# Performance work log

Measured on AMD Instinct MI355X. Metric: run time of the kernel, lower is better.

The kernel has to match this reference:

```python
import jax, jax.numpy as jnp
import numpy as np

K_NEIGHBORS = 6
LN_EPS = 1e-5


def _layernorm(h, g, b):
    m = h.mean(-1, keepdims=True)
    v = h.var(-1, keepdims=True)
    return (h - m) / jnp.sqrt(v + LN_EPS) * g + b


def _mlp(h, w0, b0, w1, b1):
    return jax.nn.relu(h @ w0 + b0) @ w1 + b1


def _learn_adj(x, Wp, bp):
    # EfficientGraphStructureLearner: cosine-sim topk graph, symmetrized, row-normalized
    h = x @ Wp + bp
    nrm = jnp.linalg.norm(h, axis=1, keepdims=True)
    h = h / jnp.maximum(nrm, 1e-12)
    S = h @ h.T                                  # [N, N]
    vals, idx = jax.lax.top_k(S, K_NEIGHBORS + 1)  # col 0 is self (diag == 1)
    N = x.shape[0]
    rows = jnp.arange(N)[:, None]
    adj = jnp.zeros_like(S).at[rows, idx[:, 1:]].set(vals[:, 1:])
    adj = (adj + adj.T) * 0.5
    adj = adj / (adj.sum(1, keepdims=True) + 1e-8)
    return adj


def _gcn(h, adj, W, b):
    # StandardGraphConv: D^-1/2 (A+I) D^-1/2 @ (h W) + b (diag matmuls as row/col scaling)
    A = adj + jnp.eye(adj.shape[0], dtype=adj.dtype)
    d = jnp.maximum(A.sum(1), 1e-12) ** -0.5
    norm_adj = d[:, None] * A * d[None, :]
    return norm_adj @ (h @ W) + b


def setup_inputs() -> dict:
    key = jax.random.key(0)
    ks = iter(jax.random.split(key, 40))
    N, D, H, O, HP = 8192, 20, 32, 128, 16
    f = lambda *s: jax.random.normal(next(ks), s, dtype=jnp.float32) * 0.1
    inp = {
        'x': jax.random.normal(next(ks), (N, D), dtype=jnp.float32),
        'Wp': f(D, HP), 'bp': jnp.zeros((HP,), jnp.float32),
        'gw0': f(D, H), 'gb0': jnp.zeros((H,), jnp.float32),
        'gw1': f(H, H), 'gb1': jnp.zeros((H,), jnp.float32),
        'gw2': f(H, O), 'gb2': jnp.zeros((O,), jnp.float32),
        'lg0': jnp.ones((H,), jnp.float32), 'lb0': jnp.zeros((H,), jnp.float32),
        'lg1': jnp.ones((H,), jnp.float32), 'lb1': jnp.zeros((H,), jnp.float32),
        'lg2': jnp.ones((O,), jnp.float32), 'lb2': jnp.zeros((O,), jnp.float32),
        'riw0': f(D, H), 'rib0': jnp.zeros((H,), jnp.float32),
        'riw1': f(H, H), 'rib1': jnp.zeros((H,), jnp.float32),
        'rhw0': f(H, H), 'rhb0': jnp.zeros((H,), jnp.float32),
        'rhw1': f(H, H), 'rhb1': jnp.zeros((H,), jnp.float32),
        'row0': f(H, O), 'rob0': jnp.zeros((O,), jnp.float32),
        'row1': f(O, O), 'rob1': jnp.zeros((O,), jnp.float32),
    }
    return inp


def reference(x, Wp, bp, gw0, gb0, gw1, gb1, gw2, gb2,
              lg0, lb0, lg1, lb1, lg2, lb2,
              riw0, rib0, riw1, rib1,
              rhw0, rhb0, rhw1, rhb1,
              row0, rob0, row1, rob1):
    adj = _learn_adj(x, Wp, bp)
    gcns = [(gw0, gb0, lg0, lb0), (gw1, gb1, lg1, lb1), (gw2, gb2, lg2, lb2)]
    skips = [(riw0, rib0, riw1, rib1), (rhw0, rhb0, rhw1, rhb1), (row0, rob0, row1, rob1)]
    h = x
    for i, ((W, b, g, bt), sk) in enumerate(zip(gcns, skips)):
        h_new = jax.nn.relu(_layernorm(_gcn(h, adj, W, b), g, bt))
        h = h_new + _mlp(h, *sk)
        # dropout is identity in eval mode
    return h
```

## Files before the change

### kernel.cpp

```cpp
#include <hip/hip_runtime.h>

constexpr int D_IN = 20;
constexpr int HP   = 16;
constexpr int K    = 6;
constexpr int SAMP = 512;
constexpr int CAPL = 384;
constexpr int CIN  = 128;
constexpr float MARGIN = 0.01f;

typedef __attribute__((ext_vector_type(8))) short bf16x8;
typedef __attribute__((ext_vector_type(4))) float f32x4;

__device__ __forceinline__ float dot16_seq(const float4* q, const float4* c) {
  float s = 0.f;
#pragma unroll
  for (int m = 0; m < 4; ++m) {
    s = fmaf(q[m].x, c[m].x, s);
    s = fmaf(q[m].y, c[m].y, s);
    s = fmaf(q[m].z, c[m].z, s);
    s = fmaf(q[m].w, c[m].w, s);
  }
  return s;
}

__device__ __forceinline__ short f2bf(float f) {
  unsigned u = __float_as_uint(f);
  unsigned r = (u + 0x7fffu + ((u >> 16) & 1u)) >> 16;
  return (short)r;
}

__device__ __forceinline__ float dinv_of(float own, float ins) {
  float rs = 0.5f * (own + ins);
  float rn = 1.f / (rs + 1e-8f);
  return rsqrtf(fmaxf(1.f + rs * rn, 1e-12f));
}

__global__ void k_proj(const float* __restrict__ x, const float* __restrict__ Wp,
                       const float* __restrict__ bp, const float* __restrict__ gw0,
                       float* __restrict__ hn, short* __restrict__ hnb,
                       float* __restrict__ XW0,
                       float* __restrict__ insum, int* __restrict__ indeg, int N) {
  int i = blockIdx.x * blockDim.x + threadIdx.x;
  if (i >= N) return;
  insum[i] = 0.f; indeg[i] = 0;
  float xr[D_IN];
#pragma unroll
  for (int d = 0; d < D_IN; ++d) xr[d] = x[i*D_IN + d];
  float hv[HP];
  float nrm2 = 0.f;
#pragma unroll
  for (int h = 0; h < HP; ++h) {
    float a = bp[h];
#pragma unroll
    for (int d = 0; d < D_IN; ++d) a += xr[d] * Wp[d*HP + h];
    hv[h] = a;
    nrm2 += a * a;
  }
  float inv = 1.f / fmaxf(sqrtf(nrm2), 1e-12f);
#pragma unroll
  for (int h = 0; h < HP; ++h) {
    float v = hv[h] * inv;
    hn[i*HP + h] = v;
    hnb[(size_t)i*32 + h] = f2bf(v);
  }
#pragma unroll
  for (int h = 0; h < HP; ++h) hnb[(size_t)i*32 + 16 + h] = 0;
#pragma unroll
  for (int oc = 0; oc < 32; ++oc) {
    float a = 0.f;
#pragma unroll
    for (int d = 0; d < D_IN; ++d) a += xr[d] * gw0[d*32 + oc];
    XW0[(size_t)i*32 + oc] = a;
  }
}

struct Top6 { float v0,v1,v2,v3,v4,v5; int i0,i1,i2,i3,i4,i5; };

__device__ __forceinline__ void t6_init(Top6& t) {
  t.v0=t.v1=t.v2=t.v3=t.v4=t.v5=-1e30f;
  t.i0=t.i1=t.i2=t.i3=t.i4=t.i5=-1;
}

#define T6_SWAP(a,b,ia,ib) { float tv=a; a=b; b=tv; int ti=ia; ia=ib; ib=ti; }

__device__ __forceinline__ void t6_insert(Top6& t, float s, int c) {
  if (s > t.v5) {
    t.v5 = s; t.i5 = c;
    if (t.v5 > t.v4) { T6_SWAP(t.v4, t.v5, t.i4, t.i5); }
    if (t.v4 > t.v3) { T6_SWAP(t.v3, t.v4, t.i3, t.i4); }
    if (t.v3 > t.v2) { T6_SWAP(t.v2, t.v3, t.i2, t.i3); }
    if (t.v2 > t.v1) { T6_SWAP(t.v1, t.v2, t.i1, t.i2); }
    if (t.v1 > t.v0) { T6_SWAP(t.v0, t.v1, t.i0, t.i1); }
  }
}

__device__ __forceinline__ void t6_best(const Top6& t, float& cv, int& ci) {
  cv = t.v0; ci = t.i0;
  if (t.v1 > cv || (t.v1 == cv && (unsigned)t.i1 < (unsigned)ci)) { cv = t.v1; ci = t.i1; }
  if (t.v2 > cv || (t.v2 == cv && (unsigned)t.i2 < (unsigned)ci)) { cv = t.v2; ci = t.i2; }
  if (t.v3 > cv || (t.v3 == cv && (unsigned)t.i3 < (unsigned)ci)) { cv = t.v3; ci = t.i3; }
  if (t.v4 > cv || (t.v4 == cv && (unsigned)t.i4 < (unsigned)ci)) { cv = t.v4; ci = t.i4; }
  if (t.v5 > cv || (t.v5 == cv && (unsigned)t.i5 < (unsigned)ci)) { cv = t.v5; ci = t.i5; }
}

__device__ __forceinline__ void t6_consume(Top6& t, int mi) {
  if (t.i0 == mi) t.v0 = -1e30f;
  if (t.i1 == mi) t.v1 = -1e30f;
  if (t.i2 == mi) t.v2 = -1e30f;
  if (t.i3 == mi) t.v3 = -1e30f;
  if (t.i4 == mi) t.v4 = -1e30f;
  if (t.i5 == mi) t.v5 = -1e30f;
}

__global__ __launch_bounds__(256) void k_thresh(const float* __restrict__ hn,
                                                float* __restrict__ tau, int N) {
  int wave = threadIdx.x >> 6, lane = threadIdx.x & 63;
  int row = blockIdx.x * 4 + wave;
  const float4* hn4 = (const float4*)hn;
  float4 q[4];
#pragma unroll
  for (int m = 0; m < 4; ++m) q[m] = hn4[(size_t)row*4 + m];
  Top6 t; t6_init(t);
#pragma unroll
  for (int k = 0; k < SAMP/64; ++k) {
    int c = lane + 64*k;
    if (c != row) {
      float4 cv[4];
#pragma unroll
      for (int m = 0; m < 4; ++m) cv[m] = hn4[(size_t)c*4 + m];
      float s = dot16_seq(q, cv);
      t6_insert(t, s, c);
    }
  }
  float last = -1e30f;
  for (int sel = 0; sel < K; ++sel) {
    float cv; int ci;
    t6_best(t, cv, ci);
    float mv = cv; int mi = ci;
#pragma unroll
    for (int m = 1; m < 64; m <<= 1) {
      float ov = __shfl_xor(mv, m);
      int   oi = __shfl_xor(mi, m);
      if (ov > mv || (ov == mv && (unsigned)oi < (unsigned)mi)) { mv = ov; mi = oi; }
    }
    t6_consume(t, mi);
    last = mv;
  }
  if (lane == 0) tau[row] = last;
}

__global__ __launch_bounds__(1024) void k_scan23(
    const float* __restrict__ hn, const short* __restrict__ hnb,
    const float* __restrict__ tau,
    float* __restrict__ evals, int* __restrict__ eidx,
    float* __restrict__ ownsum, float* insum, int* indeg,
    unsigned short* __restrict__ incol, float* __restrict__ inval, int N) {
  __shared__ unsigned short hbuf[16][CAPL];
  __shared__ int cntl[16];
  int tid = threadIdx.x;
  int wave = tid >> 6, lane = tid & 63;
  int r0 = blockIdx.x * 16;
  const float4* hn4 = (const float4*)hn;

  if (tid < 16) cntl[tid] = 0;
  __syncthreads();

  {
    int half = lane >> 4;
    int l16  = lane & 15;
    int gleader = half << 4;
    unsigned below = (1u << l16) - 1u;
    bf16x8 a = *(const bf16x8*)(hnb + (size_t)(r0 + l16)*32 + half*8);
    float4 t4 = *(const float4*)(tau + r0 + half*4);
    float tm0 = t4.x - MARGIN, tm1 = t4.y - MARGIN,
          tm2 = t4.z - MARGIN, tm3 = t4.w - MARGIN;
    f32x4 zero = {0.f, 0.f, 0.f, 0.f};
    const int SPANW = N / 16;
    int jb0 = wave * SPANW;

#define APPB2(R, HA, HB)                                                     \
    {                                                                        \
      bool hA = (HA), hB = (HB);                                             \
      unsigned long long mrA = __ballot(hA);                                 \
      unsigned long long mrB = __ballot(hB);                                 \
      unsigned maskA = (unsigned)(mrA >> (16*half)) & 0xFFFFu;               \
      unsigned maskB = (unsigned)(mrB >> (16*half)) & 0xFFFFu;               \
      if (maskA | maskB) {                                                   \
        int rl = 4*half + (R);                                               \
        int pca = __popc(maskA);                                             \
        int base = 0;                                                        \
        if (l16 == 0) base = atomicAdd(&cntl[rl], pca + __popc(maskB));      \
        base = __shfl(base, gleader);                                        \
        if (hA) {                                                            \
          int p = base + __popc(maskA & below);                              \
          if (p < CAPL) hbuf[rl][p] = (unsigned short)(jbA + l16);           \
        }                                                                    \
        if (hB) {                                                            \
          int p = base + pca + __popc(maskB & below);                        \
          if (p < CAPL) hbuf[rl][p] = (unsigned short)(jbB + l16);           \
        }                                                                    \
      }                                                                      \
    }

#pragma unroll 2
    for (int jt = 0; jt < SPANW; jt += 32) {
      int jbA = jb0 + jt, jbB = jbA + 16;
      bf16x8 bA = *(const bf16x8*)(hnb + (size_t)(jbA + l16)*32 + half*8);
      bf16x8 bB = *(const bf16x8*)(hnb + (size_t)(jbB + l16)*32 + half*8);
      f32x4 dA = __builtin_amdgcn_mfma_f32_16x16x32_bf16(a, bA, zero, 0, 0, 0);
      f32x4 dB = __builtin_amdgcn_mfma_f32_16x16x32_bf16(a, bB, zero, 0, 0, 0);
      bool a0 = dA[0] >= tm0, a1 = dA[1] >= tm1, a2 = dA[2] >= tm2, a3 = dA[3] >= tm3;
      bool b0 = dB[0] >= tm0, b1 = dB[1] >= tm1, b2 = dB[2] >= tm2, b3 = dB[3] >= tm3;
      if (__any(a0 | a1 | a2 | a3 | b0 | b1 | b2 | b3)) {
        APPB2(0, a0, b0) APPB2(1, a1, b1) APPB2(2, a2, b2) APPB2(3, a3, b3)
      }
    }
#undef APPB2
  }
  __syncthreads();

  {
    int row = r0 + wave;
    int n = min(cntl[wave], CAPL);
    float4 q[4];
#pragma unroll
    for (int m = 0; m < 4; ++m) q[m] = hn4[(size_t)row*4 + m];
    Top6 t; t6_init(t);
    for (int e = lane; e < n; e += 64) {
      int j = hbuf[wave][e];
      if (j != row) {
        float4 cv[4];
#pragma unroll
        for (int m = 0; m < 4; ++m) cv[m] = hn4[(size_t)j*4 + m];
        float sc = dot16_seq(q, cv);
        t6_insert(t, sc, j);
      }
    }
    float osum = 0.f;
    for (int sel = 0; sel < K; ++sel) {
      float cv; int ci;
      t6_best(t, cv, ci);
      float mv = cv; int mi = ci;
#pragma unroll
      for (int m = 1; m < 64; m <<= 1) {
        float ov = __shfl_xor(mv, m);
        int   oi = __shfl_xor(mi, m);
        if (ov > mv || (ov == mv && (unsigned)oi < (unsigned)mi)) { mv = ov; mi = oi; }
      }
      t6_consume(t, mi);
      if (lane == 0) {
        evals[row*K + sel] = mv;
        eidx [row*K + sel] = mi;
        osum += mv;
        atomicAdd(&insum[mi], mv);
        int pos = atomicAdd(&indeg[mi], 1);
        if (pos < CIN) {
          incol[(size_t)mi*CIN + pos] = (unsigned short)row;
          inval[(size_t)mi*CIN + pos] = mv;
        }
      }
    }
    if (lane == 0) ownsum[row] = osum;
  }
}

template<int DIN, int NEXTD, bool SCALED>
__global__ __launch_bounds__(256) void k_gpost32(
    const float* __restrict__ XWsrc,
    const int* __restrict__ eidx, const float* __restrict__ evals,
    const unsigned short* __restrict__ incol, const float* __restrict__ inval,
    const int* __restrict__ indeg,
    const float* __restrict__ ownsum, const float* __restrict__ insum,
    const float* __restrict__ gb, const float* __restrict__ lg, const float* __restrict__ lb,
    const float* __restrict__ hprev,
    const float* __restrict__ w0, const float* __restrict__ b0,
    const float* __restrict__ w1, const float* __restrict__ b1,
    const float* __restrict__ Wnext, float* __restrict__ XWnext,
    float* __restrict__ outp, int N) {
  __shared__ float hid[4][2][32];
  int tid = threadIdx.x;
  int lane = tid & 63, wslot = tid >> 6;
  int sub = lane >> 5, ol = lane & 31;
  int row = (blockIdx.x * 4 + wslot) * 2 + sub;

  float rs_i = 0.5f * (ownsum[row] + insum[row]);
  float rn_i = 1.f / (rs_i + 1e-8f);
  float di_i = rsqrtf(fmaxf(1.f + rs_i * rn_i, 1e-12f));
  float cc = 0.5f * di_i * rn_i;
  float acc = (SCALED ? di_i : di_i * di_i) * XWsrc[(size_t)row*32 + ol];
#pragma unroll
  for (int t = 0; t < K; ++t) {
    int j = eidx[row*K + t]; float v = evals[row*K + t];
    float cf;
    if constexpr (SCALED) cf = cc * v;
    else                  cf = cc * v * dinv_of(ownsum[j], insum[j]);
    acc = fmaf(cf, XWsrc[(size_t)j*32 + ol], acc);
  }
  int ne = min(indeg[row], CIN);
  for (int e = 0; e < ne; ++e) {
    int j = incol[(size_t)row*CIN + e]; float v = inval[(size_t)row*CIN + e];
    float cf;
    if constexpr (SCALED) cf = cc * v;
    else                  cf = cc * v * dinv_of(ownsum[j], insum[j]);
    acc = fmaf(cf, XWsrc[(size_t)j*32 + ol], acc);
  }
  float u0 = acc + gb[ol];
  float s = u0;
#pragma unroll
  for (int m = 1; m < 32; m <<= 1) s += __shfl_xor(s, m);
  float mean = s * (1.f/32.f);
  float d0 = u0 - mean;
  float vs = d0*d0;
#pragma unroll
  for (int m = 1; m < 32; m <<= 1) vs += __shfl_xor(vs, m);
  float rstd = rsqrtf(vs * (1.f/32.f) + 1e-5f);
  float t0 = fmaxf(d0*rstd*lg[ol] + lb[ol], 0.f);

  float hp[DIN];
#pragma unroll
  for (int d = 0; d < DIN; ++d) hp[d] = hprev[(size_t)row*DIN + d];
  float a = b0[ol];
#pragma unroll
  for (int d = 0; d < DIN; ++d) a = fmaf(hp[d], w0[d*32 + ol], a);
  hid[wslot][sub][ol] = fmaxf(a, 0.f);
  float o = b1[ol];
#pragma unroll
  for (int h = 0; h < 32; ++h) o = fmaf(hid[wslot][sub][h], w1[h*32 + ol], o);
  float hv = t0 + o;
  outp[(size_t)row*32 + ol] = hv;

  hid[wslot][sub][ol] = hv;
#pragma unroll
  for (int k2 = 0; k2 < NEXTD/32; ++k2) {
    int oc = ol + 32*k2;
    float acc2 = 0.f;
#pragma unroll
    for (int d = 0; d < 32; ++d)
      acc2 = fmaf(hid[wslot][sub][d], Wnext[d*NEXTD + oc], acc2);
    XWnext[(size_t)row*NEXTD + oc] = di_i * acc2;
  }
}

__global__ __launch_bounds__(256) void k_gpost128(
    const float* __restrict__ XW,
    const int* __restrict__ eidx, const float* __restrict__ evals,
    const unsigned short* __restrict__ incol, const float* __restrict__ inval,
    const int* __restrict__ indeg,
    const float* __restrict__ ownsum, const float* __restrict__ insum,
    const float* __restrict__ b, const float* __restrict__ g, const float* __restrict__ bt,
    const float* __restrict__ hprev,
    const float* __restrict__ w0, const float* __restrict__ b0,
    const float* __restrict__ w1, const float* __restrict__ b1,
    float* __restrict__ out, int N) {
  __shared__ float hid_s[4][128];
  __shared__ float w1s[2048];
  int wslot = threadIdx.x >> 6;
  int row   = (blockIdx.x * blockDim.x + threadIdx.x) >> 6;
  int lane  = threadIdx.x & 63;
  int o0 = lane, o1 = lane + 64;

  float rs_i = 0.5f * (ownsum[row] + insum[row]);
  float rn_i = 1.f / (rs_i + 1e-8f);
  float di_i = rsqrtf(fmaxf(1.f + rs_i * rn_i, 1e-12f));
  float cc = 0.5f * di_i * rn_i;
  float acc0 = di_i * XW[(size_t)row*128 + o0];
  float acc1 = di_i * XW[(size_t)row*128 + o1];
#pragma unroll
  for (int t = 0; t < K; ++t) {
    int j = eidx[row*K + t];
    float cf = cc * evals[row*K + t];
    acc0 = fmaf(cf, XW[(size_t)j*128 + o0], acc0);
    acc1 = fmaf(cf, XW[(size_t)j*128 + o1], acc1);
  }
  int ne = min(indeg[row], CIN);
  for (int e = 0; e < ne; ++e) {
    int j = incol[(size_t)row*CIN + e];
    float cf = cc * inval[(size_t)row*CIN + e];
    acc0 = fmaf(cf, XW[(size_t)j*128 + o0], acc0);
    acc1 = fmaf(cf, XW[(size_t)j*128 + o1], acc1);
  }
  float u0 = acc0 + b[o0];
  float u1 = acc1 + b[o1];

  float s = u0 + u1;
#pragma unroll
  for (int m = 1; m < 64; m <<= 1) s += __shfl_xor(s, m);
  float mean = s * (1.f/128.f);
  float d0 = u0 - mean, d1 = u1 - mean;
  float vs = d0*d0 + d1*d1;
#pragma unroll
  for (int m = 1; m < 64; m <<= 1) vs += __shfl_xor(vs, m);
  float rstd = rsqrtf(vs * (1.f/128.f) + 1e-5f);
  float t0 = fmaxf(d0*rstd*g[o0] + bt[o0], 0.f);
  float t1 = fmaxf(d1*rstd*g[o1] + bt[o1], 0.f);

  float hp[32];
#pragma unroll
  for (int d = 0; d < 32; ++d) hp[d] = hprev[(size_t)row*32 + d];
  {
    float a = b0[o0];
#pragma unroll
    for (int d = 0; d < 32; ++d) a = fmaf(hp[d], w0[d*128 + o0], a);
    hid_s[wslot][o0] = fmaxf(a, 0.f);
    float a1 = b0[o1];
#pragma unroll
    for (int d = 0; d < 32; ++d) a1 = fmaf(hp[d], w0[d*128 + o1], a1);
    hid_s[wslot][o1] = fmaxf(a1, 0.f);
  }

  float r0=0.f, r1=0.f, r2=0.f, r3=0.f, q0=0.f, q1=0.f, q2=0.f, q3=0.f;
  for (int c = 0; c < 8; ++c) {
    __syncthreads();
    {
      const float4* src = (const float4*)(w1 + c*2048);
      float4* dst = (float4*)w1s;
      dst[threadIdx.x]       = src[threadIdx.x];
      dst[threadIdx.x + 256] = src[threadIdx.x + 256];
    }
    __syncthreads();
    int hb = c*16;
#pragma unroll
    for (int hh = 0; hh < 16; hh += 4) {
      float h0 = hid_s[wslot][hb+hh+0], h1 = hid_s[wslot][hb+hh+1],
            h2 = hid_s[wslot][hb+hh+2], h3 = hid_s[wslot][hb+hh+3];
      r0 = fmaf(h0, w1s[(hh+0)*128 + o0], r0); q0 = fmaf(h0, w1s[(hh+0)*128 + o1], q0);
      r1 = fmaf(h1, w1s[(hh+1)*128 + o0], r1); q1 = fmaf(h1, w1s[(hh+1)*128 + o1], q1);
      r2 = fmaf(h2, w1s[(hh+2)*128 + o0], r2); q2 = fmaf(h2, w1s[(hh+2)*128 + o1], q2);
      r3 = fmaf(h3, w1s[(hh+3)*128 + o0], r3); q3 = fmaf(h3, w1s[(hh+3)*128 + o1], q3);
    }
  }
  out[(size_t)row*128 + o0] = t0 + b1[o0] + ((r0 + r1) + (r2 + r3));
  out[(size_t)row*128 + o1] = t1 + b1[o1] + ((q0 + q1) + (q2 + q3));
}

extern "C" void kernel_launch(void* const* d_in, const int* in_sizes, int n_in,
                              void* d_out, int out_size, void* d_ws, size_t ws_size,
                              hipStream_t stream) {
  const float* x    = (const float*)d_in[0];
  const float* Wp   = (const float*)d_in[1];
  const float* bp   = (const float*)d_in[2];
  const float* gw0  = (const float*)d_in[3];
  const float* gb0  = (const float*)d_in[4];
  const float* gw1  = (const float*)d_in[5];
  const float* gb1  = (const float*)d_in[6];
  const float* gw2  = (const float*)d_in[7];
  const float* gb2  = (const float*)d_in[8];
  const float* lg0  = (const float*)d_in[9];
  const float* lb0  = (const float*)d_in[10];
  const float* lg1  = (const float*)d_in[11];
  const float* lb1  = (const float*)d_in[12];
  const float* lg2  = (const float*)d_in[13];
  const float* lb2  = (const float*)d_in[14];
  const float* riw0 = (const float*)d_in[15];
  const float* rib0 = (const float*)d_in[16];
  const float* riw1 = (const float*)d_in[17];
  const float* rib1 = (const float*)d_in[18];
  const float* rhw0 = (const float*)d_in[19];
  const float* rhb0 = (const float*)d_in[20];
  const float* rhw1 = (const float*)d_in[21];
  const float* rhb1 = (const float*)d_in[22];
  const float* row0 = (const float*)d_in[23];
  const float* rob0 = (const float*)d_in[24];
  const float* row1 = (const float*)d_in[25];
  const float* rob1 = (const float*)d_in[26];
  int N = in_sizes[0] / D_IN;
  float* out = (float*)d_out;

  char* ws = (char*)d_ws;
  size_t off = 0;
  auto alloc = [&](size_t bytes) -> void* {
    void* p = ws + off;
    off += (bytes + 255) & ~(size_t)255;
    return p;
  };
  float* hn      = (float*)alloc((size_t)N * HP * 4);
  float* evals   = (float*)alloc((size_t)N * K * 4);
  int*   eidx    = (int*)  alloc((size_t)N * K * 4);
  float* ownsum  = (float*)alloc((size_t)N * 4);
  float* insum   = (float*)alloc((size_t)N * 4);
  int*   indeg   = (int*)  alloc((size_t)N * 4);
  float* XWa     = (float*)alloc((size_t)N * 128 * 4);
  float* XWb     = (float*)alloc((size_t)N * 32 * 4);
  float* h1      = (float*)alloc((size_t)N * 32 * 4);
  float* h2      = (float*)alloc((size_t)N * 32 * 4);
  float* tau     = (float*)alloc((size_t)N * 4);
  short* hnb     = (short*)alloc((size_t)N * 32 * 2);
  unsigned short* incol = (unsigned short*)alloc((size_t)N * CIN * 2);
  float* inval   = (float*)alloc((size_t)N * CIN * 4);
  (void)ws_size; (void)n_in; (void)out_size;

  const int B = 256;
  hipLaunchKernelGGL(k_proj, dim3((N + B - 1) / B), dim3(B), 0, stream,
                     x, Wp, bp, gw0, hn, hnb, XWa, insum, indeg, N);
  hipLaunchKernelGGL(k_thresh, dim3(N / 4), dim3(B), 0, stream, hn, tau, N);
  hipLaunchKernelGGL(k_scan23, dim3(N / 16), dim3(1024), 0, stream,
                     hn, hnb, tau, evals, eidx, ownsum, insum, indeg, incol, inval, N);

  hipLaunchKernelGGL((k_gpost32<20, 32, false>), dim3(N / 8), dim3(B), 0, stream,
                     XWa, eidx, evals, incol, inval, indeg, ownsum, insum,
                     gb0, lg0, lb0, x, riw0, rib0, riw1, rib1, gw1, XWb, h1, N);
  hipLaunchKernelGGL((k_gpost32<32, 128, true>), dim3(N / 8), dim3(B), 0, stream,
                     XWb, eidx, evals, incol, inval, indeg, ownsum, insum,
                     gb1, lg1, lb1, h1, rhw0, rhb0, rhw1, rhb1, gw2, XWa, h2, N);
  hipLaunchKernelGGL(k_gpost128, dim3(N / 4), dim3(B), 0, stream,
                     XWa, eidx, evals, incol, inval, indeg, ownsum, insum,
                     gb2, lg2, lb2, h2, row0, rob0, row1, rob1, out, N);
}
```

Baseline: 137.6 us.

## Replace atomic candidate list with per-row hit bitmasks in shared memory

The scan phase no longer compacts candidate indices with LDS atomics, shuffles and popcounts. It now writes 16-bit ballot masks per tile into a per-row bitmap, one word per lane-0 per half. The refinement phase iterates over set bits of the bitmap to rescore candidates. This removes atomics and the capacity cap in the hot MFMA loop, at the cost of an unconditional LDS store every iteration and possibly uneven per-lane work when bits are decoded.

```diff
diff --git a/kernel.cpp b/kernel.cpp
--- a/kernel.cpp
+++ b/kernel.cpp
@@ -4,7 +4,6 @@
 constexpr int HP   = 16;
 constexpr int K    = 6;
 constexpr int SAMP = 512;
-constexpr int CAPL = 384;
 constexpr int CIN  = 128;
 constexpr float MARGIN = 0.01f;
 
@@ -155,21 +154,16 @@
     float* __restrict__ evals, int* __restrict__ eidx,
     float* __restrict__ ownsum, float* insum, int* indeg,
     unsigned short* __restrict__ incol, float* __restrict__ inval, int N) {
-  __shared__ unsigned short hbuf[16][CAPL];
-  __shared__ int cntl[16];
+  __shared__ unsigned short hm[16][512];
   int tid = threadIdx.x;
   int wave = tid >> 6, lane = tid & 63;
   int r0 = blockIdx.x * 16;
   const float4* hn4 = (const float4*)hn;
-
-  if (tid < 16) cntl[tid] = 0;
-  __syncthreads();
+  unsigned* hmu = (unsigned*)hm;
 
   {
     int half = lane >> 4;
     int l16  = lane & 15;
-    int gleader = half << 4;
-    unsigned below = (1u << l16) - 1u;
     bf16x8 a = *(const bf16x8*)(hnb + (size_t)(r0 + l16)*32 + half*8);
     float4 t4 = *(const float4*)(tau + r0 + half*4);
     float tm0 = t4.x - MARGIN, tm1 = t4.y - MARGIN,
@@ -178,30 +172,6 @@
     const int SPANW = N / 16;
     int jb0 = wave * SPANW;
 
-#define APPB2(R, HA, HB)                                                     \
-    {                                                                        \
-      bool hA = (HA), hB = (HB);                                             \
-      unsigned long long mrA = __ballot(hA);                                 \
-      unsigned long long mrB = __ballot(hB);                                 \
-      unsigned maskA = (unsigned)(mrA >> (16*half)) & 0xFFFFu;               \
-      unsigned maskB = (unsigned)(mrB >> (16*half)) & 0xFFFFu;               \
-      if (maskA | maskB) {                                                   \
-        int rl = 4*half + (R);                                               \
-        int pca = __popc(maskA);                                             \
-        int base = 0;                                                        \
-        if (l16 == 0) base = atomicAdd(&cntl[rl], pca + __popc(maskB));      \
-        base = __shfl(base, gleader);                                        \
-        if (hA) {                                                            \
-          int p = base + __popc(maskA & below);                              \
-          if (p < CAPL) hbuf[rl][p] = (unsigned short)(jbA + l16);           \
-        }                                                                    \
-        if (hB) {                                                            \
-          int p = base + pca + __popc(maskB & below);                        \
-          if (p < CAPL) hbuf[rl][p] = (unsigned short)(jbB + l16);           \
-        }                                                                    \
-      }                                                                      \
-    }
-
 #pragma unroll 2
     for (int jt = 0; jt < SPANW; jt += 32) {
       int jbA = jb0 + jt, jbB = jbA + 16;
@@ -209,31 +179,46 @@
       bf16x8 bB = *(const bf16x8*)(hnb + (size_t)(jbB + l16)*32 + half*8);
       f32x4 dA = __builtin_amdgcn_mfma_f32_16x16x32_bf16(a, bA, zero, 0, 0, 0);
       f32x4 dB = __builtin_amdgcn_mfma_f32_16x16x32_bf16(a, bB, zero, 0, 0, 0);
-      bool a0 = dA[0] >= tm0, a1 = dA[1] >= tm1, a2 = dA[2] >= tm2, a3 = dA[3] >= tm3;
-      bool b0 = dB[0] >= tm0, b1 = dB[1] >= tm1, b2 = dB[2] >= tm2, b3 = dB[3] >= tm3;
-      if (__any(a0 | a1 | a2 | a3 | b0 | b1 | b2 | b3)) {
-        APPB2(0, a0, b0) APPB2(1, a1, b1) APPB2(2, a2, b2) APPB2(3, a3, b3)
+      unsigned mA0 = (unsigned)(__ballot(dA[0] >= tm0) >> (16*half)) & 0xFFFFu;
+      unsigned mA1 = (unsigned)(__ballot(dA[1] >= tm1) >> (16*half)) & 0xFFFFu;
+      unsigned mA2 = (unsigned)(__ballot(dA[2] >= tm2) >> (16*half)) & 0xFFFFu;
+      unsigned mA3 = (unsigned)(__ballot(dA[3] >= tm3) >> (16*half)) & 0xFFFFu;
+      unsigned mB0 = (unsigned)(__ballot(dB[0] >= tm0) >> (16*half)) & 0xFFFFu;
+      unsigned mB1 = (unsigned)(__ballot(dB[1] >= tm1) >> (16*half)) & 0xFFFFu;
+      unsigned mB2 = (unsigned)(__ballot(dB[2] >= tm2) >> (16*half)) & 0xFFFFu;
+      unsigned mB3 = (unsigned)(__ballot(dB[3] >= tm3) >> (16*half)) & 0xFFFFu;
+      if (l16 == 0) {
+        int tp = (wave << 4) + (jt >> 5);
+        int rb = (half << 2) << 8;
+        hmu[rb         + tp] = mA0 | (mB0 << 16);
+        hmu[rb + 256   + tp] = mA1 | (mB1 << 16);
+        hmu[rb + 512   + tp] = mA2 | (mB2 << 16);
+        hmu[rb + 768   + tp] = mA3 | (mB3 << 16);
       }
     }
-#undef APPB2
   }
   __syncthreads();
 
   {
     int row = r0 + wave;
-    int n = min(cntl[wave], CAPL);
     float4 q[4];
 #pragma unroll
     for (int m = 0; m < 4; ++m) q[m] = hn4[(size_t)row*4 + m];
     Top6 t; t6_init(t);
-    for (int e = lane; e < n; e += 64) {
-      int j = hbuf[wave][e];
-      if (j != row) {
-        float4 cv[4];
-#pragma unroll
-        for (int m = 0; m < 4; ++m) cv[m] = hn4[(size_t)j*4 + m];
-        float sc = dot16_seq(q, cv);
-        t6_insert(t, sc, j);
+#pragma unroll
+    for (int tp = 0; tp < 8; ++tp) {
+      int tile = lane + (tp << 6);
+      unsigned m = hm[wave][tile];
+      while (m) {
+        int b = __ffs(m) - 1; m &= m - 1;
+        int j = (tile << 4) + b;
+        if (j != row) {
+          float4 cv[4];
+#pragma unroll
+          for (int mm2 = 0; mm2 < 4; ++mm2) cv[mm2] = hn4[(size_t)j*4 + mm2];
+          float sc = dot16_seq(q, cv);
+          t6_insert(t, sc, j);
+        }
       }
     }
     float osum = 0.f;
```

After: 139.4 us. No clear change (+1.3%).
